# Kernel optimization log

Hardware: AMD Instinct MI355X
Metric: run time of the kernel (lower is better)

Reference implementation:

```python
import jax, jax.numpy as jnp
import numpy as np

NUM_QUBITS = 4
SHOTS = 1000
BATCH = 8192
IN_SIZE = 4096
OUT_SIZE = 4096


def setup_inputs() -> dict:
    key = jax.random.key(0)
    k_x, k_w, k_b, k_q = jax.random.split(key, 4)
    x = jax.random.normal(k_x, (BATCH, IN_SIZE), dtype=jnp.float32)
    W = jax.random.normal(k_w, (OUT_SIZE, IN_SIZE), dtype=jnp.float32) * (1.0 / np.sqrt(IN_SIZE))
    b = jax.random.normal(k_b, (OUT_SIZE,), dtype=jnp.float32) * 0.01
    # Each shot's measurement outcome: num_qubits independent uniform bits
    # == one uniform integer in [0, 2**num_qubits).
    quantum_outcomes = jax.random.randint(k_q, (BATCH, SHOTS), 0, 2 ** NUM_QUBITS, dtype=jnp.int32)
    return {"x": x, "W": W, "b": b, "quantum_outcomes": quantum_outcomes}


def reference(x, W, b, quantum_outcomes):
    # classical path: nn.Linear
    classical = jnp.einsum("bi,oi->bo", x, W) + b  # [B, OUT]
    # normalized by max outcome, broadcast across the output dim.
    max_outcome = float(2 ** NUM_QUBITS - 1)
    expectation = jnp.mean(quantum_outcomes.astype(jnp.float32), axis=1) / max_outcome  # [B]
    return classical + expectation[:, None]
```

## Files before the change

kernel.cpp:

```cpp
#include <hip/hip_runtime.h>
#include <hip/hip_bf16.h>

typedef __attribute__((ext_vector_type(8))) short short8;
typedef __attribute__((ext_vector_type(4))) float f32x4;
typedef unsigned short ushort_t;

#define BM 128
#define BN 128
#define BK 64

__device__ __forceinline__ ushort_t f2bf_rne(float f) {
    unsigned u = __float_as_uint(f);
    u += 0x7FFF + ((u >> 16) & 1);
    return (ushort_t)(u >> 16);
}

__global__ void expect_kernel(const int* __restrict__ q, float* __restrict__ e,
                              int rows, int shots) {
    int row = blockIdx.x * (blockDim.x >> 6) + (threadIdx.x >> 6);
    int lane = threadIdx.x & 63;
    if (row >= rows) return;
    const int* rp = q + (long long)row * shots;
    int s = 0;
    for (int j = lane; j < shots; j += 64) s += rp[j];
    #pragma unroll
    for (int off = 32; off; off >>= 1) s += __shfl_down(s, off, 64);
    if (lane == 0) e[row] = (float)s * (1.0f / (1000.0f * 15.0f));
}

__global__ void cvt_kernel(const float* __restrict__ src, ushort_t* __restrict__ dst,
                           long long n4) {
    long long i = (long long)blockIdx.x * blockDim.x + threadIdx.x;
    if (i >= n4) return;
    float4 v = ((const float4*)src)[i];
    ushort4 o;
    o.x = f2bf_rne(v.x); o.y = f2bf_rne(v.y);
    o.z = f2bf_rne(v.z); o.w = f2bf_rne(v.w);
    ((ushort4*)dst)[i] = o;
}

__global__ __launch_bounds__(256, 2)
void gemm_kernel(const ushort_t* __restrict__ A, const ushort_t* __restrict__ B,
                 const float* __restrict__ bias, const float* __restrict__ expect,
                 float* __restrict__ C, int M, int N, int K) {
    __shared__ ushort_t As[BM * BK];
    __shared__ ushort_t Bs[BN * BK];

    const int num_pid_n = N / BN;
    const int GROUP = 8;
    int pid = blockIdx.x;
    int group_size = GROUP * num_pid_n;
    int gid = pid / group_size;
    int pin = pid - gid * group_size;
    int pid_m = gid * GROUP + (pin % GROUP);
    int pid_n = pin / GROUP;

    const int tid  = threadIdx.x;
    const int lane = tid & 63;
    const int wave = tid >> 6;
    const int wm = (wave >> 1) * 64;
    const int wn = (wave & 1) * 64;

    const int srow = tid >> 3;
    const int scol = (tid & 7) * 8;

    const ushort_t* a_ptr = A + (long long)pid_m * BM * K + scol;
    const ushort_t* b_ptr = B + (long long)pid_n * BN * K + scol;

    f32x4 acc[4][4];
    #pragma unroll
    for (int i = 0; i < 4; i++)
        #pragma unroll
        for (int j = 0; j < 4; j++)
            acc[i][j] = (f32x4)(0.0f);

    const int quad = lane >> 4;
    const int l15  = lane & 15;

    for (int k0 = 0; k0 < K; k0 += BK) {
        #pragma unroll
        for (int s = 0; s < 4; s++) {
            int row = srow + s * 32;
            __builtin_amdgcn_global_load_lds(
                (const __attribute__((address_space(1))) unsigned int*)(a_ptr + (long long)row * K + k0),
                (__attribute__((address_space(3))) unsigned int*)(As + row * BK + scol),
                16, 0, 0);
        }
        #pragma unroll
        for (int s = 0; s < 4; s++) {
            int row = srow + s * 32;
            __builtin_amdgcn_global_load_lds(
                (const __attribute__((address_space(1))) unsigned int*)(b_ptr + (long long)row * K + k0),
                (__attribute__((address_space(3))) unsigned int*)(Bs + row * BK + scol),
                16, 0, 0);
        }
        __syncthreads();

        #pragma unroll
        for (int ks = 0; ks < 2; ks++) {
            int ko = ks * 32 + quad * 8;
            short8 af[4], bf[4];
            #pragma unroll
            for (int i = 0; i < 4; i++) {
                af[i] = *(const short8*)(As + (wm + i * 16 + l15) * BK + ko);
                bf[i] = *(const short8*)(Bs + (wn + i * 16 + l15) * BK + ko);
            }
            #pragma unroll
            for (int i = 0; i < 4; i++)
                #pragma unroll
                for (int j = 0; j < 4; j++)
                    acc[i][j] = __builtin_amdgcn_mfma_f32_16x16x32_bf16(
                        af[i], bf[j], acc[i][j], 0, 0, 0);
        }
        __syncthreads();
    }

    long long row0 = (long long)pid_m * BM + wm;
    int col0 = pid_n * BN + wn;
    #pragma unroll
    for (int j = 0; j < 4; j++) {
        int col = col0 + j * 16 + l15;
        float bj = bias[col];
        #pragma unroll
        for (int i = 0; i < 4; i++) {
            #pragma unroll
            for (int r = 0; r < 4; r++) {
                long long row = row0 + i * 16 + quad * 4 + r;
                C[row * N + col] = acc[i][j][r] + bj + expect[row];
            }
        }
    }
}

__device__ __forceinline__ short8 pack8(float4 a, float4 b) {
    short8 r;
    r[0] = (short)f2bf_rne(a.x); r[1] = (short)f2bf_rne(a.y);
    r[2] = (short)f2bf_rne(a.z); r[3] = (short)f2bf_rne(a.w);
    r[4] = (short)f2bf_rne(b.x); r[5] = (short)f2bf_rne(b.y);
    r[6] = (short)f2bf_rne(b.z); r[7] = (short)f2bf_rne(b.w);
    return r;
}

__global__ __launch_bounds__(256, 2)
void gemm_f32stage_kernel(const float* __restrict__ A, const float* __restrict__ B,
                          const float* __restrict__ bias, const float* __restrict__ expect,
                          float* __restrict__ C, int M, int N, int K) {
    __shared__ ushort_t As[BM * BK];
    __shared__ ushort_t Bs[BN * BK];

    const int num_pid_n = N / BN;
    const int GROUP = 8;
    int pid = blockIdx.x;
    int group_size = GROUP * num_pid_n;
    int gid = pid / group_size;
    int pin = pid - gid * group_size;
    int pid_m = gid * GROUP + (pin % GROUP);
    int pid_n = pin / GROUP;

    const int tid  = threadIdx.x;
    const int lane = tid & 63;
    const int wave = tid >> 6;
    const int wm = (wave >> 1) * 64;
    const int wn = (wave & 1) * 64;

    const int srow = tid >> 1;
    const int shalf = (tid & 1) * 32;

    const float* a_base = A + ((long long)pid_m * BM + srow) * K + shalf;
    const float* b_base = B + ((long long)pid_n * BN + srow) * K + shalf;

    f32x4 acc[4][4];
    #pragma unroll
    for (int i = 0; i < 4; i++)
        #pragma unroll
        for (int j = 0; j < 4; j++)
            acc[i][j] = (f32x4)(0.0f);

    const int quad = lane >> 4;
    const int l15  = lane & 15;

    for (int k0 = 0; k0 < K; k0 += BK) {
        {
            const float4* ap = (const float4*)(a_base + k0);
            const float4* bp = (const float4*)(b_base + k0);
            float4 fa[8], fb[8];
            #pragma unroll
            for (int c = 0; c < 8; c++) { fa[c] = ap[c]; fb[c] = bp[c]; }
            #pragma unroll
            for (int c = 0; c < 4; c++) {
                *(short8*)(As + srow * BK + shalf + c * 8) = pack8(fa[2*c], fa[2*c+1]);
                *(short8*)(Bs + srow * BK + shalf + c * 8) = pack8(fb[2*c], fb[2*c+1]);
            }
        }
        __syncthreads();

        #pragma unroll
        for (int ks = 0; ks < 2; ks++) {
            int ko = ks * 32 + quad * 8;
            short8 af[4], bf[4];
            #pragma unroll
            for (int i = 0; i < 4; i++) {
                af[i] = *(const short8*)(As + (wm + i * 16 + l15) * BK + ko);
                bf[i] = *(const short8*)(Bs + (wn + i * 16 + l15) * BK + ko);
            }
            #pragma unroll
            for (int i = 0; i < 4; i++)
                #pragma unroll
                for (int j = 0; j < 4; j++)
                    acc[i][j] = __builtin_amdgcn_mfma_f32_16x16x32_bf16(
                        af[i], bf[j], acc[i][j], 0, 0, 0);
        }
        __syncthreads();
    }

    long long row0 = (long long)pid_m * BM + wm;
    int col0 = pid_n * BN + wn;
    #pragma unroll
    for (int j = 0; j < 4; j++) {
        int col = col0 + j * 16 + l15;
        float bj = bias[col];
        #pragma unroll
        for (int i = 0; i < 4; i++) {
            #pragma unroll
            for (int r = 0; r < 4; r++) {
                long long row = row0 + i * 16 + quad * 4 + r;
                C[row * N + col] = acc[i][j][r] + bj + expect[row];
            }
        }
    }
}

extern "C" void kernel_launch(void* const* d_in, const int* in_sizes, int n_in,
                              void* d_out, int out_size, void* d_ws, size_t ws_size,
                              hipStream_t stream) {
    const float* x = (const float*)d_in[0];
    const float* W = (const float*)d_in[1];
    const float* b = (const float*)d_in[2];
    const int*   q = (const int*)d_in[3];
    float* out = (float*)d_out;

    const int M = 8192, N = 4096, K = 4096, SHOTS = 1000;

    float* expect = (float*)d_ws;
    size_t need = 32768 + (size_t)M * K * 2 + (size_t)N * K * 2;

    expect_kernel<<<M / 4, 256, 0, stream>>>(q, expect, M, SHOTS);

    if (ws_size >= need) {
        ushort_t* xb = (ushort_t*)((char*)d_ws + 32768);
        ushort_t* wb = xb + (size_t)M * K;
        cvt_kernel<<<(int)((long long)M * K / 4 / 256), 256, 0, stream>>>(x, xb, (long long)M * K / 4);
        cvt_kernel<<<(int)((long long)N * K / 4 / 256), 256, 0, stream>>>(W, wb, (long long)N * K / 4);
        gemm_kernel<<<(M / BM) * (N / BN), 256, 0, stream>>>(xb, wb, b, expect, out, M, N, K);
    } else {
        gemm_f32stage_kernel<<<(M / BM) * (N / BN), 256, 0, stream>>>(x, W, b, expect, out, M, N, K);
    }
}
```

Measured before the change: 614.2 us.

## XOR-swizzle LDS tiles in GEMM and fuse bf16 conversion kernels

```diff
diff --git a/kernel.cpp b/kernel.cpp
--- a/kernel.cpp
+++ b/kernel.cpp
@@ -28,15 +28,28 @@
     if (lane == 0) e[row] = (float)s * (1.0f / (1000.0f * 15.0f));
 }
 
-__global__ void cvt_kernel(const float* __restrict__ src, ushort_t* __restrict__ dst,
-                           long long n4) {
-    long long i = (long long)blockIdx.x * blockDim.x + threadIdx.x;
-    if (i >= n4) return;
-    float4 v = ((const float4*)src)[i];
-    ushort4 o;
-    o.x = f2bf_rne(v.x); o.y = f2bf_rne(v.y);
-    o.z = f2bf_rne(v.z); o.w = f2bf_rne(v.w);
-    ((ushort4*)dst)[i] = o;
+__device__ __forceinline__ short8 pack8(float4 a, float4 b) {
+    short8 r;
+    r[0] = (short)f2bf_rne(a.x); r[1] = (short)f2bf_rne(a.y);
+    r[2] = (short)f2bf_rne(a.z); r[3] = (short)f2bf_rne(a.w);
+    r[4] = (short)f2bf_rne(b.x); r[5] = (short)f2bf_rne(b.y);
+    r[6] = (short)f2bf_rne(b.z); r[7] = (short)f2bf_rne(b.w);
+    return r;
+}
+
+__global__ void cvt2_kernel(const float* __restrict__ x, ushort_t* __restrict__ xb,
+                            const float* __restrict__ w, ushort_t* __restrict__ wb,
+                            int blocks_x) {
+    const float* src; ushort_t* dst; long long base;
+    if (blockIdx.x < blocks_x) {
+        src = x; dst = xb; base = (long long)blockIdx.x * blockDim.x;
+    } else {
+        src = w; dst = wb; base = (long long)(blockIdx.x - blocks_x) * blockDim.x;
+    }
+    long long i = base + threadIdx.x;
+    float4 a = ((const float4*)src)[2 * i];
+    float4 b = ((const float4*)src)[2 * i + 1];
+    ((short8*)dst)[i] = pack8(a, b);
 }
 
 __global__ __launch_bounds__(256, 2)
@@ -62,10 +75,11 @@
     const int wn = (wave & 1) * 64;
 
     const int srow = tid >> 3;
-    const int scol = (tid & 7) * 8;
-
-    const ushort_t* a_ptr = A + (long long)pid_m * BM * K + scol;
-    const ushort_t* b_ptr = B + (long long)pid_n * BN * K + scol;
+    const int slot = tid & 7;
+    const int gchunk = slot ^ (srow & 7);
+
+    const ushort_t* a_ptr = A + (long long)pid_m * BM * K + gchunk * 8;
+    const ushort_t* b_ptr = B + (long long)pid_n * BN * K + gchunk * 8;
 
     f32x4 acc[4][4];
     #pragma unroll
@@ -76,6 +90,7 @@
 
     const int quad = lane >> 4;
     const int l15  = lane & 15;
+    const int rlow = l15 & 7;
 
     for (int k0 = 0; k0 < K; k0 += BK) {
         #pragma unroll
@@ -83,7 +98,7 @@
             int row = srow + s * 32;
             __builtin_amdgcn_global_load_lds(
                 (const __attribute__((address_space(1))) unsigned int*)(a_ptr + (long long)row * K + k0),
-                (__attribute__((address_space(3))) unsigned int*)(As + row * BK + scol),
+                (__attribute__((address_space(3))) unsigned int*)(As + row * BK + slot * 8),
                 16, 0, 0);
         }
         #pragma unroll
@@ -91,19 +106,20 @@
             int row = srow + s * 32;
             __builtin_amdgcn_global_load_lds(
                 (const __attribute__((address_space(1))) unsigned int*)(b_ptr + (long long)row * K + k0),
-                (__attribute__((address_space(3))) unsigned int*)(Bs + row * BK + scol),
+                (__attribute__((address_space(3))) unsigned int*)(Bs + row * BK + slot * 8),
                 16, 0, 0);
         }
         __syncthreads();
 
         #pragma unroll
         for (int ks = 0; ks < 2; ks++) {
-            int ko = ks * 32 + quad * 8;
+            int q = ks * 4 + quad;
+            int sw = (q ^ rlow) * 8;
             short8 af[4], bf[4];
             #pragma unroll
             for (int i = 0; i < 4; i++) {
-                af[i] = *(const short8*)(As + (wm + i * 16 + l15) * BK + ko);
-                bf[i] = *(const short8*)(Bs + (wn + i * 16 + l15) * BK + ko);
+                af[i] = *(const short8*)(As + (wm + i * 16 + l15) * BK + sw);
+                bf[i] = *(const short8*)(Bs + (wn + i * 16 + l15) * BK + sw);
             }
             #pragma unroll
             for (int i = 0; i < 4; i++)
@@ -130,15 +146,6 @@
             }
         }
     }
-}
-
-__device__ __forceinline__ short8 pack8(float4 a, float4 b) {
-    short8 r;
-    r[0] = (short)f2bf_rne(a.x); r[1] = (short)f2bf_rne(a.y);
-    r[2] = (short)f2bf_rne(a.z); r[3] = (short)f2bf_rne(a.w);
-    r[4] = (short)f2bf_rne(b.x); r[5] = (short)f2bf_rne(b.y);
-    r[6] = (short)f2bf_rne(b.z); r[7] = (short)f2bf_rne(b.w);
-    return r;
 }
 
 __global__ __launch_bounds__(256, 2)
@@ -164,10 +171,10 @@
     const int wn = (wave & 1) * 64;
 
     const int srow = tid >> 1;
-    const int shalf = (tid & 1) * 32;
-
-    const float* a_base = A + ((long long)pid_m * BM + srow) * K + shalf;
-    const float* b_base = B + ((long long)pid_n * BN + srow) * K + shalf;
+    const int chalf = (tid & 1) * 4;
+
+    const float* a_base = A + ((long long)pid_m * BM + srow) * K + chalf * 8;
+    const float* b_base = B + ((long long)pid_n * BN + srow) * K + chalf * 8;
 
     f32x4 acc[4][4];
     #pragma unroll
@@ -178,6 +185,7 @@
 
     const int quad = lane >> 4;
     const int l15  = lane & 15;
+    const int rlow = l15 & 7;
 
     for (int k0 = 0; k0 < K; k0 += BK) {
         {
@@ -188,20 +196,22 @@
             for (int c = 0; c < 8; c++) { fa[c] = ap[c]; fb[c] = bp[c]; }
             #pragma unroll
             for (int c = 0; c < 4; c++) {
-                *(short8*)(As + srow * BK + shalf + c * 8) = pack8(fa[2*c], fa[2*c+1]);
-                *(short8*)(Bs + srow * BK + shalf + c * 8) = pack8(fb[2*c], fb[2*c+1]);
+                int sl = ((chalf + c) ^ (srow & 7)) * 8;
+                *(short8*)(As + srow * BK + sl) = pack8(fa[2*c], fa[2*c+1]);
+                *(short8*)(Bs + srow * BK + sl) = pack8(fb[2*c], fb[2*c+1]);
             }
         }
         __syncthreads();
 
         #pragma unroll
         for (int ks = 0; ks < 2; ks++) {
-            int ko = ks * 32 + quad * 8;
+            int q = ks * 4 + quad;
+            int sw = (q ^ rlow) * 8;
             short8 af[4], bf[4];
             #pragma unroll
             for (int i = 0; i < 4; i++) {
-                af[i] = *(const short8*)(As + (wm + i * 16 + l15) * BK + ko);
-                bf[i] = *(const short8*)(Bs + (wn + i * 16 + l15) * BK + ko);
+                af[i] = *(const short8*)(As + (wm + i * 16 + l15) * BK + sw);
+                bf[i] = *(const short8*)(Bs + (wn + i * 16 + l15) * BK + sw);
             }
             #pragma unroll
             for (int i = 0; i < 4; i++)
@@ -249,8 +259,9 @@
     if (ws_size >= need) {
         ushort_t* xb = (ushort_t*)((char*)d_ws + 32768);
         ushort_t* wb = xb + (size_t)M * K;
-        cvt_kernel<<<(int)((long long)M * K / 4 / 256), 256, 0, stream>>>(x, xb, (long long)M * K / 4);
-        cvt_kernel<<<(int)((long long)N * K / 4 / 256), 256, 0, stream>>>(W, wb, (long long)N * K / 4);
+        int blocks_x = (int)((long long)M * K / 8 / 256);
+        int blocks_w = (int)((long long)N * K / 8 / 256);
+        cvt2_kernel<<<blocks_x + blocks_w, 256, 0, stream>>>(x, xb, W, wb, blocks_x);
         gemm_kernel<<<(M / BM) * (N / BN), 256, 0, stream>>>(xb, wb, b, expect, out, M, N, K);
     } else {
         gemm_f32stage_kernel<<<(M / BM) * (N / BN), 256, 0, stream>>>(x, W, b, expect, out, M, N, K);
```

Measured after the change: 589.8 us. -4.0%, faster.
